# Optimization experiments

Hardware: AMD Instinct MI355X
Metric: run time of the kernel (lower is better)

## Reference

```python
import jax, jax.numpy as jnp
import numpy as np

NHID = 128
NLAYERS = 4
DT = 1.0
ALPHA = 1.0
GAMMA = 1.0


def setup_inputs() -> dict:
    key = jax.random.key(0)
    k1, k2, k3, k4, k5, k6 = jax.random.split(key, 6)
    N, E = 100000, 1600000
    stdv = 1.0 / np.sqrt(NHID)
    x = jax.random.normal(k1, (N, NHID), dtype=jnp.float32)
    edge_index = jax.random.randint(k2, (2, E), 0, N, dtype=jnp.int64)
    # GCNConv.lin weight (no bias) and separate conv bias; reset_params uniform(-stdv, stdv) for weights
    W = jax.random.uniform(k3, (NHID, NHID), jnp.float32, -stdv, stdv)
    b = jnp.zeros((NHID,), jnp.float32)
    Wres = jax.random.uniform(k4, (NHID, NHID), jnp.float32, -stdv, stdv)
    bres = jax.random.uniform(k5, (NHID,), jnp.float32, -stdv, stdv)
    return {"x": x, "edge_index": edge_index, "W": W, "b": b, "Wres": Wres, "bres": bres}


def reference(x, edge_index, W, b, Wres, bres):
    N = x.shape[0]
    src, dst = edge_index[0], edge_index[1]
    # GCN degree normalization with self-loops (A_hat = A + I)
    deg = jax.ops.segment_sum(jnp.ones(src.shape[0], x.dtype), dst, num_segments=N) + 1.0
    dinv = jax.lax.rsqrt(deg)  # deg >= 1 from self-loops

    def conv(X):
        h = X @ W  # lin (no bias)
        norm = (dinv[src] * dinv[dst])[:, None]
        msg = h[src] * norm                      # [E, nhid] gather
        agg = jax.ops.segment_sum(msg, dst, num_segments=N)  # scatter-add
        agg = agg + h * (dinv * dinv)[:, None]   # self-loop contribution
        return agg + b

    def residual(X):
        # res_connection_v1: -res(conv.lin(X))
        return -((X @ W) @ Wres + bres)

    # dropout is identity in eval mode
    Y = jnp.tanh(x)
    X = Y
    for _ in range(NLAYERS):
        Y = Y + DT * (jnp.tanh(conv(X) + residual(X)) - ALPHA * Y - GAMMA * X)
        X = X + DT * Y
    return X
```

## Files before the change

kernel.cpp:

```cpp
#include <hip/hip_runtime.h>
#include <hip/hip_bf16.h>
#include <stdint.h>

#define THREADS 256
#define WB 256
#define MAXNB 512
#define NBLK_A 512

typedef unsigned short u16;
typedef unsigned int u32;
using frag_ab = __attribute__((ext_vector_type(8))) short;
using f32x4  = __attribute__((ext_vector_type(4))) float;

static __host__ __device__ inline int imin(int a, int b) { return a < b ? a : b; }

static __device__ inline u16 f2b(float f) {
    u32 u = __builtin_bit_cast(u32, f);
    return (u16)((u + 0x7FFFu + ((u >> 16) & 1u)) >> 16);
}
static __device__ inline float b2f_lo(u32 v) { return __builtin_bit_cast(float, v << 16); }
static __device__ inline float b2f_hi(u32 v) { return __builtin_bit_cast(float, v & 0xFFFF0000u); }

static __device__ inline float tanh_fast(float x) {
    const float e = __builtin_amdgcn_exp2f(x * 2.8853900817779268f);
    return 1.0f - 2.0f * __builtin_amdgcn_rcpf(e + 1.0f);
}

static __device__ inline void fma8(float* a, float w, uint4 v) {
    a[0] = fmaf(w, b2f_lo(v.x), a[0]); a[1] = fmaf(w, b2f_hi(v.x), a[1]);
    a[2] = fmaf(w, b2f_lo(v.y), a[2]); a[3] = fmaf(w, b2f_hi(v.y), a[3]);
    a[4] = fmaf(w, b2f_lo(v.z), a[4]); a[5] = fmaf(w, b2f_hi(v.z), a[5]);
    a[6] = fmaf(w, b2f_lo(v.w), a[6]); a[7] = fmaf(w, b2f_hi(v.w), a[7]);
}

static __device__ inline bool detect64(const int* raw) {
    __shared__ int s64;
    if (threadIdx.x == 0) s64 = 1;
    __syncthreads();
    if (raw[2 * threadIdx.x + 1] != 0) s64 = 0;
    __syncthreads();
    return s64 != 0;
}

__global__ __launch_bounds__(256)
void k_bucket_count(const int* __restrict__ raw, int E, int EPB, int NB,
                    int* __restrict__ counts) {
    const bool is64 = detect64(raw);
    __shared__ int cnt[MAXNB];
    const int t = threadIdx.x, blk = blockIdx.x;
    for (int i = t; i < NB; i += THREADS) cnt[i] = 0;
    __syncthreads();
    const int e0 = blk * EPB, e1 = imin(E, e0 + EPB);
    for (int e = e0 + t; e < e1; e += THREADS) {
        const int d = is64 ? raw[2 * E + 2 * e] : raw[E + e];
        atomicAdd(&cnt[d >> 8], 1);
    }
    __syncthreads();
    for (int i = t; i < NB; i += THREADS) counts[i * NBLK_A + blk] = cnt[i];
}

__global__ void k_chunk_sums(const int* __restrict__ a, int* __restrict__ chunkSum, int L) {
    __shared__ int sm[THREADS];
    const int base = blockIdx.x * 2048 + threadIdx.x * 8;
    int s = 0;
#pragma unroll
    for (int i = 0; i < 8; ++i) { int idx = base + i; if (idx < L) s += a[idx]; }
    sm[threadIdx.x] = s;
    __syncthreads();
    for (int off = THREADS / 2; off > 0; off >>= 1) {
        if (threadIdx.x < off) sm[threadIdx.x] += sm[threadIdx.x + off];
        __syncthreads();
    }
    if (threadIdx.x == 0) chunkSum[blockIdx.x] = sm[0];
}

__global__ void k_scan_offsets(const int* __restrict__ chunkSum, int* __restrict__ chunkOff,
                               int nChunks) {
    if (blockIdx.x == 0 && threadIdx.x == 0) {
        int run = 0;
        for (int i = 0; i < nChunks; ++i) { chunkOff[i] = run; run += chunkSum[i]; }
    }
}

__global__ void k_scan_write(int* __restrict__ a, const int* __restrict__ chunkOff, int L) {
    __shared__ int sm[THREADS];
    const int tid = threadIdx.x;
    const int base = blockIdx.x * 2048 + tid * 8;
    int v[8]; int s = 0;
#pragma unroll
    for (int i = 0; i < 8; ++i) { int idx = base + i; v[i] = (idx < L) ? a[idx] : 0; s += v[i]; }
    const int mysum = s;
    sm[tid] = s;
    __syncthreads();
    for (int off = 1; off < THREADS; off <<= 1) {
        int t = (tid >= off) ? sm[tid - off] : 0;
        __syncthreads();
        sm[tid] += t;
        __syncthreads();
    }
    int run = chunkOff[blockIdx.x] + sm[tid] - mysum;
#pragma unroll
    for (int i = 0; i < 8; ++i) {
        int idx = base + i;
        if (idx < L) { a[idx] = run; run += v[i]; }
    }
}

__global__ __launch_bounds__(256)
void k_bucket_scatter(const int* __restrict__ raw, int E, int EPB, int NB,
                      const int* __restrict__ offs, u32* __restrict__ pairs) {
    const bool is64 = detect64(raw);
    __shared__ int cur[MAXNB];
    const int t = threadIdx.x, blk = blockIdx.x;
    for (int i = t; i < NB; i += THREADS) cur[i] = offs[i * NBLK_A + blk];
    __syncthreads();
    const int e0 = blk * EPB, e1 = imin(E, e0 + EPB);
    for (int e = e0 + t; e < e1; e += THREADS) {
        int s, d;
        if (is64) { s = raw[2 * e]; d = raw[2 * E + 2 * e]; }
        else      { s = raw[e];     d = raw[E + e]; }
        const int p = atomicAdd(&cur[d >> 8], 1);
        pairs[p] = (u32)s | ((u32)(d & 255) << 24);
    }
}

__global__ __launch_bounds__(256)
void k_build(const u32* __restrict__ pairs, const int* __restrict__ offs,
             int* __restrict__ rowptrP, int* __restrict__ perm, int* __restrict__ csr_src,
             float* __restrict__ dinv, int N, int NB, int E) {
    __shared__ int deg[WB];
    __shared__ int rnk[WB];
    __shared__ int degR[WB];
    __shared__ int scanR[WB];
    __shared__ int cur[WB];
    const int k = blockIdx.x, t = threadIdx.x;
    const int base = offs[k * NBLK_A];
    const int end  = (k + 1 < NB) ? offs[(k + 1) * NBLK_A] : E;
    const int n0 = k * WB;
    deg[t] = 0;
    __syncthreads();
    for (int e = base + t; e < end; e += THREADS)
        atomicAdd(&deg[pairs[e] >> 24], 1);
    __syncthreads();
    const int dv = deg[t];
    if (n0 + t < N) dinv[n0 + t] = rsqrtf((float)dv + 1.0f);
    int r = 0;
    for (int u = 0; u < WB; ++u) {
        const int du = deg[u];
        r += (du < dv) || (du == dv && u < t);
    }
    rnk[t] = r;
    degR[r] = dv;
    __syncthreads();
    scanR[t] = degR[t];
    __syncthreads();
    for (int off = 1; off < WB; off <<= 1) {
        int v = (t >= off) ? scanR[t - off] : 0;
        __syncthreads();
        scanR[t] += v;
        __syncthreads();
    }
    rowptrP[k * WB + t] = base + scanR[t] - degR[t];
    if (k == NB - 1 && t == 0) rowptrP[NB * WB] = E;
    perm[k * WB + r] = (n0 + t < N) ? (n0 + t) : -1;
    cur[t] = base + scanR[r] - dv;
    __syncthreads();
    for (int e = base + t; e < end; e += THREADS) {
        const u32 w = pairs[e];
        const int p = atomicAdd(&cur[w >> 24], 1);
        csr_src[p] = (int)(w & 0xFFFFFF);
    }
}

__global__ void k_wfill(const int* __restrict__ csr_src, const float* __restrict__ dinv,
                        uint2* __restrict__ csrW, int E) {
    int i = blockIdx.x * blockDim.x + threadIdx.x;
    const int st = gridDim.x * blockDim.x;
    for (; i < E; i += st) {
        const int s = csr_src[i];
        csrW[i] = make_uint2((u32)s, __builtin_bit_cast(u32, dinv[s]));
    }
}

__global__ void k_w2(const float* __restrict__ W, const float* __restrict__ Wres,
                     const float* __restrict__ b, const float* __restrict__ bres,
                     u16* __restrict__ Bt, float* __restrict__ cvec) {
    const int gid = blockIdx.x * blockDim.x + threadIdx.x;
    if (gid < 128 * 128) {
        const int i = gid >> 7, n = gid & 127;
        float s = 0.f;
#pragma unroll 8
        for (int k = 0; k < 128; ++k) s += W[i * 128 + k] * Wres[k * 128 + n];
        Bt[n * 256 + 128 + i] = f2b(-s);
        Bt[n * 256 + i]       = f2b(W[i * 128 + n]);
    }
    if (gid < 128) cvec[gid] = b[gid] - bres[gid];
}

__global__ void k_tanh0(const float* __restrict__ x, u16* __restrict__ Xh, long long n4) {
    long long i = blockIdx.x * (long long)blockDim.x + threadIdx.x;
    const long long stride = gridDim.x * (long long)blockDim.x;
    for (; i < n4; i += stride) {
        float4 v = ((const float4*)x)[i];
        u32 lo = f2b(tanh_fast(v.x)) | ((u32)f2b(tanh_fast(v.y)) << 16);
        u32 hi = f2b(tanh_fast(v.z)) | ((u32)f2b(tanh_fast(v.w)) << 16);
        ((uint2*)Xh)[i] = make_uint2(lo, hi);
    }
}

__global__ __launch_bounds__(256)
void k_agg(const u16* __restrict__ Xh, const int* __restrict__ rowptrP,
           const int* __restrict__ perm, const uint2* __restrict__ csrW,
           u16* __restrict__ Ph) {
    const int qid = threadIdx.x >> 4;
    const int l16 = threadIdx.x & 15;
    const int g = blockIdx.x * 16 + qid;
    const int node = perm[g];
    const int e0 = rowptrP[g], e1 = rowptrP[g + 1];
    const int c8 = l16 * 8;
    const float dn = rsqrtf((float)(e1 - e0) + 1.0f);
    float acc[8] = {0.f, 0.f, 0.f, 0.f, 0.f, 0.f, 0.f, 0.f};
    if (node >= 0) {
        const uint4 v = *(const uint4*)&Xh[(size_t)node * 128 + c8];
        fma8(acc, dn, v);
    }
    int e = e0;
    if (e + 8 <= e1) {
        uint2 cw[8];
#pragma unroll
        for (int i = 0; i < 8; ++i) cw[i] = csrW[e + i];
        while (true) {
            uint4 v[8];
#pragma unroll
            for (int i = 0; i < 8; ++i)
                v[i] = *(const uint4*)&Xh[(size_t)cw[i].x * 128 + c8];
            e += 8;
            const bool more = (e + 8 <= e1);
            uint2 nw[8];
            if (more) {
#pragma unroll
                for (int i = 0; i < 8; ++i) nw[i] = csrW[e + i];
            }
#pragma unroll
            for (int i = 0; i < 8; ++i)
                fma8(acc, __builtin_bit_cast(float, cw[i].y), v[i]);
            if (!more) break;
#pragma unroll
            for (int i = 0; i < 8; ++i) cw[i] = nw[i];
        }
    }
    for (; e < e1; ++e) {
        const uint2 cw = csrW[e];
        const uint4 v = *(const uint4*)&Xh[(size_t)cw.x * 128 + c8];
        fma8(acc, __builtin_bit_cast(float, cw.y), v);
    }
    if (node >= 0) {
        u32 w0 = (u32)f2b(acc[0] * dn) | ((u32)f2b(acc[1] * dn) << 16);
        u32 w1 = (u32)f2b(acc[2] * dn) | ((u32)f2b(acc[3] * dn) << 16);
        u32 w2 = (u32)f2b(acc[4] * dn) | ((u32)f2b(acc[5] * dn) << 16);
        u32 w3 = (u32)f2b(acc[6] * dn) | ((u32)f2b(acc[7] * dn) << 16);
        *(uint4*)&Ph[(size_t)node * 128 + c8] = make_uint4(w0, w1, w2, w3);
    }
}

__global__ __launch_bounds__(256)
void k_gemm_mfma(const u16* __restrict__ Ph, const u16* __restrict__ Xh,
                 const u16* __restrict__ Bt, const float* __restrict__ cvec,
                 float* __restrict__ Xout, u16* __restrict__ XhOut, int M, int writeF32) {
    __shared__ u16 Bs[128 * 128];
    const int tid = threadIdx.x;
    const int wid = tid >> 6, lane = tid & 63;
    const int rowbase = blockIdx.x * 128 + wid * 32;
    const int rl = lane & 15;
    const int kg = (lane >> 4) * 8;

    const int r0 = rowbase + rl;
    const size_t ar0 = (size_t)((r0      < M) ? r0      : M - 1);
    const size_t ar1 = (size_t)((r0 + 16 < M) ? r0 + 16 : M - 1);

    frag_ab a0[8], a1[8];
#pragma unroll
    for (int ks = 0; ks < 4; ++ks) {
        const int kk = ks * 32 + kg;
        a0[ks]     = *(const frag_ab*)&Ph[ar0 * 128 + kk];
        a1[ks]     = *(const frag_ab*)&Ph[ar1 * 128 + kk];
        a0[ks + 4] = *(const frag_ab*)&Xh[ar0 * 128 + kk];
        a1[ks + 4] = *(const frag_ab*)&Xh[ar1 * 128 + kk];
    }

    f32x4 acc[2][8];
#pragma unroll
    for (int i = 0; i < 2; ++i)
#pragma unroll
        for (int j = 0; j < 8; ++j) acc[i][j] = (f32x4){0.f, 0.f, 0.f, 0.f};

#pragma unroll
    for (int half = 0; half < 2; ++half) {
#pragma unroll
        for (int p = 0; p < 8; ++p) {
            const int c = p * 256 + tid;
            const int row = c >> 4, c16 = c & 15;
            const uint4 v = *(const uint4*)&Bt[row * 256 + half * 128 + c16 * 8];
            *(uint4*)&Bs[row * 128 + (((c16 * 16) ^ ((row & 7) << 4)) >> 1)] = v;
        }
        __syncthreads();
#pragma unroll
        for (int ks = 0; ks < 4; ++ks) {
            const int kb = ks * 64 + kg * 2;
#pragma unroll
            for (int nf = 0; nf < 8; ++nf) {
                const int r = nf * 16 + rl;
                const frag_ab bv = *(const frag_ab*)&Bs[r * 128 + ((kb ^ ((r & 7) << 4)) >> 1)];
                acc[0][nf] = __builtin_amdgcn_mfma_f32_16x16x32_bf16(a0[half * 4 + ks], bv,
                                                                      acc[0][nf], 0, 0, 0);
                acc[1][nf] = __builtin_amdgcn_mfma_f32_16x16x32_bf16(a1[half * 4 + ks], bv,
                                                                      acc[1][nf], 0, 0, 0);
            }
        }
        __syncthreads();
    }

    const int rq = (lane >> 4) * 4;
    if (writeF32) {
#pragma unroll
        for (int mf = 0; mf < 2; ++mf)
#pragma unroll
            for (int nf = 0; nf < 8; ++nf) {
                const int c = nf * 16 + rl;
                const float cv = cvec[c];
#pragma unroll
                for (int reg = 0; reg < 4; ++reg) {
                    const int r = rowbase + mf * 16 + rq + reg;
                    if (r < M) Xout[(size_t)r * 128 + c] = tanh_fast(acc[mf][nf][reg] + cv);
                }
            }
    } else {
#pragma unroll
        for (int mf = 0; mf < 2; ++mf)
#pragma unroll
            for (int nf = 0; nf < 8; ++nf) {
                const int c = nf * 16 + rl;
                const float cv = cvec[c];
#pragma unroll
                for (int reg = 0; reg < 4; ++reg) {
                    const int rloc = wid * 32 + mf * 16 + rq + reg;
                    Bs[rloc * 128 + (c ^ ((rloc & 7) << 3))] =
                        f2b(tanh_fast(acc[mf][nf][reg] + cv));
                }
            }
        __syncthreads();
#pragma unroll
        for (int k = 0; k < 8; ++k) {
            const int ci = k * 256 + tid;
            const int row = ci >> 4, c8 = ci & 15;
            const int gr = blockIdx.x * 128 + row;
            if (gr < M) {
                const uint4 v = *(const uint4*)&Bs[row * 128 + ((c8 * 8) ^ ((row & 7) << 3))];
                *(uint4*)&XhOut[(size_t)gr * 128 + c8 * 8] = v;
            }
        }
    }
}

extern "C" void kernel_launch(void* const* d_in, const int* in_sizes, int n_in,
                              void* d_out, int out_size, void* d_ws, size_t ws_size,
                              hipStream_t stream) {
    const float* x    = (const float*)d_in[0];
    const int*   ei   = (const int*)d_in[1];
    const float* W    = (const float*)d_in[2];
    const float* b    = (const float*)d_in[3];
    const float* Wres = (const float*)d_in[4];
    const float* bres = (const float*)d_in[5];
    const int N = in_sizes[0] / 128;
    const int E = in_sizes[1] / 2;
    float* X = (float*)d_out;

    uint8_t* base = (uint8_t*)d_ws;
    size_t off = 0;
    auto carve = [&](size_t bytes) -> void* {
        void* p = base + off;
        off += (bytes + 255) & ~(size_t)255;
        return p;
    };
    const int NB = imin((N + WB - 1) / WB, MAXNB);
    const int L = NB * NBLK_A;
    const int NPOS = NB * WB;

    u16*   Xh       = (u16*)carve((size_t)N * 128 * sizeof(u16));
    u16*   Ph       = (u16*)carve((size_t)N * 128 * sizeof(u16));
    u32*   pairs    = (u32*)carve((size_t)E * sizeof(u32));
    uint2* csrW     = (uint2*)carve((size_t)E * sizeof(uint2));
    int*   csr_src  = (int*)carve((size_t)E * sizeof(int));
    int*   counts   = (int*)carve((size_t)L * sizeof(int));
    int*   rowptrP  = (int*)carve(((size_t)NPOS + 1) * sizeof(int));
    int*   perm     = (int*)carve((size_t)NPOS * sizeof(int));
    float* dinv     = (float*)carve((size_t)N * sizeof(float));
    u16*   Bt       = (u16*)carve(128 * 256 * sizeof(u16));
    float* cvec     = (float*)carve(128 * sizeof(float));
    int*   chunkSum = (int*)carve(4096);
    int*   chunkOff = (int*)carve(4096);

    const int EPB = (E + NBLK_A - 1) / NBLK_A;
    const int nChunks = (L + 2047) / 2048;

    k_bucket_count<<<NBLK_A, THREADS, 0, stream>>>(ei, E, EPB, NB, counts);
    k_chunk_sums<<<nChunks, THREADS, 0, stream>>>(counts, chunkSum, L);
    k_scan_offsets<<<1, 64, 0, stream>>>(chunkSum, chunkOff, nChunks);
    k_scan_write<<<nChunks, THREADS, 0, stream>>>(counts, chunkOff, L);
    k_bucket_scatter<<<NBLK_A, THREADS, 0, stream>>>(ei, E, EPB, NB, counts, pairs);
    k_build<<<NB, THREADS, 0, stream>>>(pairs, counts, rowptrP, perm, csr_src, dinv, N, NB, E);
    k_wfill<<<2048, THREADS, 0, stream>>>(csr_src, dinv, csrW, E);
    k_w2<<<64, THREADS, 0, stream>>>(W, Wres, b, bres, Bt, cvec);

    const long long n4 = (long long)N * 32;
    const int tgrid = imin((int)((n4 + THREADS - 1) / THREADS), 2048);
    k_tanh0<<<tgrid, THREADS, 0, stream>>>(x, Xh, n4);

    for (int l = 0; l < 4; ++l) {
        k_agg<<<NB * 16, THREADS, 0, stream>>>(Xh, rowptrP, perm, csrW, Ph);
        k_gemm_mfma<<<(N + 127) / 128, THREADS, 0, stream>>>(Ph, Xh, Bt, cvec, X, Xh, N,
                                                             (l == 3) ? 1 : 0);
    }
}
```

Baseline: 482.1 us.

## Interleave degree-sorted nodes across aggregation blocks and shrink gather unroll

Each aggregation block now takes nodes strided across the degree-sorted 256-node window instead of a contiguous run of 16 sorted ranks, so every block gets a mix of light and heavy rows. This is meant to even out per-block work and reduce tail imbalance. The pipelined 8-wide prefetch gather loop is replaced with a simpler 4-wide unrolled loop, which lowers register pressure but gives less memory-level parallelism per thread. An unused shared array in the build kernel is also removed.

New measurement: 440.9 us. 8.5% less time.

```diff
diff --git a/kernel.cpp b/kernel.cpp
--- a/kernel.cpp
+++ b/kernel.cpp
@@ -129,7 +129,6 @@
              int* __restrict__ rowptrP, int* __restrict__ perm, int* __restrict__ csr_src,
              float* __restrict__ dinv, int N, int NB, int E) {
     __shared__ int deg[WB];
-    __shared__ int rnk[WB];
     __shared__ int degR[WB];
     __shared__ int scanR[WB];
     __shared__ int cur[WB];
@@ -149,7 +148,6 @@
         const int du = deg[u];
         r += (du < dv) || (du == dv && u < t);
     }
-    rnk[t] = r;
     degR[r] = dv;
     __syncthreads();
     scanR[t] = degR[t];
@@ -214,7 +212,10 @@
            u16* __restrict__ Ph) {
     const int qid = threadIdx.x >> 4;
     const int l16 = threadIdx.x & 15;
-    const int g = blockIdx.x * 16 + qid;
+    const int k = blockIdx.x >> 4;
+    const int j = blockIdx.x & 15;
+    const int rank = ((qid >> 2) * 16 + j) * 4 + (qid & 3);
+    const int g = k * 256 + rank;
     const int node = perm[g];
     const int e0 = rowptrP[g], e1 = rowptrP[g + 1];
     const int c8 = l16 * 8;
@@ -225,29 +226,17 @@
         fma8(acc, dn, v);
     }
     int e = e0;
-    if (e + 8 <= e1) {
-        uint2 cw[8];
-#pragma unroll
-        for (int i = 0; i < 8; ++i) cw[i] = csrW[e + i];
-        while (true) {
-            uint4 v[8];
-#pragma unroll
-            for (int i = 0; i < 8; ++i)
-                v[i] = *(const uint4*)&Xh[(size_t)cw[i].x * 128 + c8];
-            e += 8;
-            const bool more = (e + 8 <= e1);
-            uint2 nw[8];
-            if (more) {
-#pragma unroll
-                for (int i = 0; i < 8; ++i) nw[i] = csrW[e + i];
-            }
-#pragma unroll
-            for (int i = 0; i < 8; ++i)
-                fma8(acc, __builtin_bit_cast(float, cw[i].y), v[i]);
-            if (!more) break;
-#pragma unroll
-            for (int i = 0; i < 8; ++i) cw[i] = nw[i];
-        }
+    for (; e + 3 < e1; e += 4) {
+        const uint2 cw0 = csrW[e],     cw1 = csrW[e + 1];
+        const uint2 cw2 = csrW[e + 2], cw3 = csrW[e + 3];
+        const uint4 v0 = *(const uint4*)&Xh[(size_t)cw0.x * 128 + c8];
+        const uint4 v1 = *(const uint4*)&Xh[(size_t)cw1.x * 128 + c8];
+        const uint4 v2 = *(const uint4*)&Xh[(size_t)cw2.x * 128 + c8];
+        const uint4 v3 = *(const uint4*)&Xh[(size_t)cw3.x * 128 + c8];
+        fma8(acc, __builtin_bit_cast(float, cw0.y), v0);
+        fma8(acc, __builtin_bit_cast(float, cw1.y), v1);
+        fma8(acc, __builtin_bit_cast(float, cw2.y), v2);
+        fma8(acc, __builtin_bit_cast(float, cw3.y), v3);
     }
     for (; e < e1; ++e) {
         const uint2 cw = csrW[e];
```
